# Performance work log

Measured on AMD Instinct MI355X. Metric: run time of the kernel, lower is better.

Reference implementation:

```python
import jax, jax.numpy as jnp
import numpy as np

E = 1024
B, QL, KVL = 8, 2048, 2048


def setup_inputs() -> dict:
    key = jax.random.key(0)
    ks = jax.random.split(key, 12)
    s = 1.0 / np.sqrt(E)
    return {
        "query": jax.random.normal(ks[0], (B, QL, E), jnp.float32),
        "key_value": jax.random.normal(ks[1], (B, KVL, E), jnp.float32),
        "attention_mask": jax.random.randint(ks[2], (B, QL, KVL), 0, 2, jnp.int32),
        "Wq": jax.random.uniform(ks[3], (E, E), jnp.float32, -s, s),
        "bq": jax.random.uniform(ks[4], (E,), jnp.float32, -s, s),
        "Wk": jax.random.uniform(ks[5], (E, E), jnp.float32, -s, s),
        "bk": jax.random.uniform(ks[6], (E,), jnp.float32, -s, s),
        "Wv": jax.random.uniform(ks[7], (E, E), jnp.float32, -s, s),
        "bv": jax.random.uniform(ks[8], (E,), jnp.float32, -s, s),
        "Wo": jax.random.uniform(ks[9], (E, E), jnp.float32, -s, s),
        "bo": jax.random.uniform(ks[10], (E,), jnp.float32, -s, s),
    }


def reference(query, key_value, attention_mask, Wq, bq, Wk, bk, Wv, bv, Wo, bo):
    # torch Linear: x @ W.T + b
    q = jnp.einsum('bqe,fe->bqf', query, Wq) + bq          # [B, QL, E]
    k = jnp.einsum('bke,fe->bkf', key_value, Wk) + bk      # [B, KVL, E]
    v = jnp.einsum('bke,fe->bkf', key_value, Wv) + bv      # [B, KVL, E]
    scale = 1.0 / jnp.sqrt(jnp.asarray(q.shape[-1], q.dtype))
    attn = jnp.einsum('bqe,bke->bqk', q, k) * scale        # [B, QL, KVL]
    attn = jnp.where(attention_mask == 0, -jnp.inf, attn)
    attn = jax.nn.softmax(attn, axis=-1)
    out = jnp.einsum('bqk,bke->bqe', attn, v)              # [B, QL, E]
    out = jnp.einsum('bqe,fe->bqf', out, Wo) + bo
    return out
```

## Files before the change

### kernel.cpp

```cpp
#include <hip/hip_runtime.h>
#include <hip/hip_bf16.h>
#include <stdint.h>

typedef unsigned short u16;
typedef short s16x8 __attribute__((ext_vector_type(8)));
typedef u16 u16x8 __attribute__((ext_vector_type(8)));
typedef u16 u16x4 __attribute__((ext_vector_type(4)));
typedef float f32x4 __attribute__((ext_vector_type(4)));

__device__ __forceinline__ u16 f2bf(float f) {
  union { float f; uint32_t u; } c; c.f = f;
  uint32_t u = c.u;
  u = u + 0x7fffu + ((u >> 16) & 1u);
  return (u16)(u >> 16);
}
__device__ __forceinline__ float bf2f(u16 b) {
  union { uint32_t u; float f; } c; c.u = ((uint32_t)b) << 16;
  return c.f;
}

__device__ __forceinline__ void gld_lds16(const u16* g, u16* l) {
  __builtin_amdgcn_global_load_lds(
      (const __attribute__((address_space(1))) uint32_t*)g,
      (__attribute__((address_space(3))) uint32_t*)l,
      16, 0, 0);
}

__global__ __launch_bounds__(256) void cvt_f32_to_bf16(
    const float* __restrict__ in, u16* __restrict__ out, long n8) {
  long i = (long)blockIdx.x * blockDim.x + threadIdx.x;
  if (i >= n8) return;
  const float4 a = ((const float4*)in)[i * 2];
  const float4 b = ((const float4*)in)[i * 2 + 1];
  u16x8 r;
  r[0] = f2bf(a.x); r[1] = f2bf(a.y); r[2] = f2bf(a.z); r[3] = f2bf(a.w);
  r[4] = f2bf(b.x); r[5] = f2bf(b.y); r[6] = f2bf(b.z); r[7] = f2bf(b.w);
  *(u16x8*)&out[i * 8] = r;
}

__global__ __launch_bounds__(256) void cvt_w4(
    const float* __restrict__ w0, const float* __restrict__ w1,
    const float* __restrict__ w2, const float* __restrict__ w3,
    u16* __restrict__ out) {
  const float* src = (blockIdx.y == 0) ? w0 : (blockIdx.y == 1) ? w1
                   : (blockIdx.y == 2) ? w2 : w3;
  const long i = (long)blockIdx.x * blockDim.x + threadIdx.x;
  const float4 a = ((const float4*)src)[i * 2];
  const float4 b = ((const float4*)src)[i * 2 + 1];
  u16x8 r;
  r[0] = f2bf(a.x); r[1] = f2bf(a.y); r[2] = f2bf(a.z); r[3] = f2bf(a.w);
  r[4] = f2bf(b.x); r[5] = f2bf(b.y); r[6] = f2bf(b.z); r[7] = f2bf(b.w);
  *(u16x8*)&out[(long)blockIdx.y * 1048576 + i * 8] = r;
}

__global__ __launch_bounds__(256) void softmax_rows(u16* __restrict__ S) {
  const long base = (long)blockIdx.x * 2048;
  const int tid = threadIdx.x;
  const int lane = tid & 63, wave = tid >> 6;
  u16x8 raw = *(const u16x8*)&S[base + tid * 8];
  float v[8];
#pragma unroll
  for (int j = 0; j < 8; ++j) v[j] = bf2f(raw[j]);
  float m = v[0];
#pragma unroll
  for (int j = 1; j < 8; ++j) m = fmaxf(m, v[j]);
#pragma unroll
  for (int off = 32; off >= 1; off >>= 1) m = fmaxf(m, __shfl_xor(m, off));
  __shared__ float red[8];
  if (lane == 0) red[wave] = m;
  __syncthreads();
  m = fmaxf(fmaxf(red[0], red[1]), fmaxf(red[2], red[3]));
  float s = 0.f;
#pragma unroll
  for (int j = 0; j < 8; ++j) { v[j] = __expf(v[j] - m); s += v[j]; }
#pragma unroll
  for (int off = 32; off >= 1; off >>= 1) s += __shfl_xor(s, off);
  if (lane == 0) red[4 + wave] = s;
  __syncthreads();
  s = (red[4] + red[5]) + (red[6] + red[7]);
  const float inv = 1.f / s;
#pragma unroll
  for (int j = 0; j < 8; ++j) raw[j] = f2bf(v[j] * inv);
  *(u16x8*)&S[base + tid * 8] = raw;
}

union __align__(16) SmemT {
  u16 stage[2][128 * 64];
  float epi[32 * 132];
};

__device__ __forceinline__ s16x8 ldsfrag(const u16* p, int r, int c8) {
  return *(const s16x8*)&p[r * 64 + ((c8 ^ (r & 7)) << 3)];
}

__device__ __forceinline__ void stage128(const u16* __restrict__ gb, int row0,
                                         int K, int k0, u16* lbuf, int tid) {
#pragma unroll
  for (int i = 0; i < 4; ++i) {
    const int f = i * 256 + tid;
    const int rl = f >> 3, s = f & 7;
    const int gc = (s ^ (rl & 7)) << 3;
    gld_lds16(gb + (long)(row0 + rl) * K + k0 + gc, lbuf + f * 8);
  }
}

template<bool HAS_BIAS, int MODE, bool HAS_MASK>
__global__ __launch_bounds__(256, 4) void gemm128(
    const u16* __restrict__ A, const u16* __restrict__ B,
    const float* __restrict__ bias, const float* __restrict__ bias2,
    const int* __restrict__ mask, void* __restrict__ Cv,
    void* __restrict__ Cv2,
    int M, int N, int K, long sA, long sB, long sC, long sMask, float scale) {
  __shared__ SmemT sm;
  const int nx = gridDim.x, ny = gridDim.y;
  const int did = blockIdx.x + nx * (blockIdx.y + ny * blockIdx.z);
  const int cpx = (nx * ny * gridDim.z) >> 3;
  const int nf = (did & 7) * cpx + (did >> 3);
  const int b = nf / (nx * ny);
  const int rr = nf % (nx * ny);
  const int bm = (rr / ny) * 128;
  const int bn = (rr % ny) * 128;

  const u16* Ab = A + (long)b * sA;
  const u16* Bb = B + (long)b * sB;
  const int tid = threadIdx.x;
  const int lane = tid & 63, wave = tid >> 6;
  const int wm = wave >> 1, wn = wave & 1;
  const int lr = lane & 15, lk = lane >> 4;
  const int NT = K >> 6;

  f32x4 acc[4][4] = {};

  for (int t = 0; t < NT; ++t) {
    stage128(Ab, bm, K, t << 6, sm.stage[0], tid);
    stage128(Bb, bn, K, t << 6, sm.stage[1], tid);
    asm volatile("s_waitcnt vmcnt(0)" ::: "memory");
    __syncthreads();
#pragma unroll
    for (int ks = 0; ks < 2; ++ks) {
      s16x8 af[4], bg[4];
#pragma unroll
      for (int mi = 0; mi < 4; ++mi)
        af[mi] = ldsfrag(sm.stage[0], wm * 64 + mi * 16 + lr, ks * 4 + lk);
#pragma unroll
      for (int ni = 0; ni < 4; ++ni)
        bg[ni] = ldsfrag(sm.stage[1], wn * 64 + ni * 16 + lr, ks * 4 + lk);
#pragma unroll
      for (int mi = 0; mi < 4; ++mi)
#pragma unroll
        for (int ni = 0; ni < 4; ++ni)
          acc[mi][ni] = __builtin_amdgcn_mfma_f32_16x16x32_bf16(
              af[mi], bg[ni], acc[mi][ni], 0, 0, 0);
    }
    __syncthreads();
  }

  const long cb = (long)b * sC;
  if (MODE == 2 && bn >= 1024) {
#pragma unroll
    for (int mi = 0; mi < 4; ++mi) {
#pragma unroll
      for (int ni = 0; ni < 4; ++ni) {
        const int row0 = bm + wm * 64 + mi * 16 + (lk << 2);
        const int col2 = (bn - 1024) + wn * 64 + ni * 16 + lr;
        const float bvx = HAS_BIAS ? bias2[col2] : 0.f;
        u16x4 pk;
#pragma unroll
        for (int j = 0; j < 4; ++j) pk[j] = f2bf(acc[mi][ni][j] * scale + bvx);
        const long ad = (long)(row0 >> 11) * (2048L * 1024) +
                        (long)col2 * 2048 + (row0 & 2047);
        *(u16x4*)&((u16*)Cv2)[ad] = pk;
      }
    }
  } else {
    const int ldC = (MODE == 2) ? 1024 : N;
    const int q = tid & 7, r = tid >> 3;
#pragma unroll
    for (int h = 0; h < 4; ++h) {
      __syncthreads();
      if (wm == (h >> 1)) {
        const int mi0 = (h & 1) * 2;
#pragma unroll
        for (int mm = 0; mm < 2; ++mm) {
          const int mi = mi0 + mm;
#pragma unroll
          for (int ni = 0; ni < 4; ++ni) {
            const int c = wn * 64 + ni * 16 + lr;
            const float bvx = HAS_BIAS ? bias[bn + c] : 0.f;
#pragma unroll
            for (int j = 0; j < 4; ++j)
              sm.epi[(mm * 16 + (lk << 2) + j) * 132 + c] =
                  acc[mi][ni][j] * scale + bvx;
          }
        }
      }
      __syncthreads();
      const int growi = bm + h * 32 + r;
      const long grow = cb + (long)growi * ldC + bn;
      const long mrow = HAS_MASK
          ? ((long)b * sMask + (long)growi * (long)N + bn) : 0;
#pragma unroll
      for (int ch = 0; ch < 2; ++ch) {
        const int c0 = ch * 64 + q * 8;
        const float4 x = *(const float4*)&sm.epi[r * 132 + c0];
        const float4 y = *(const float4*)&sm.epi[r * 132 + c0 + 4];
        if (MODE == 1) {
          *(float4*)&((float*)Cv)[grow + c0] = x;
          *(float4*)&((float*)Cv)[grow + c0 + 4] = y;
        } else {
          u16x8 pk;
          if (HAS_MASK) {
            const int4 ma = *(const int4*)&mask[mrow + c0];
            const int4 mb = *(const int4*)&mask[mrow + c0 + 4];
            pk[0] = f2bf(ma.x ? x.x : -1e30f);
            pk[1] = f2bf(ma.y ? x.y : -1e30f);
            pk[2] = f2bf(ma.z ? x.z : -1e30f);
            pk[3] = f2bf(ma.w ? x.w : -1e30f);
            pk[4] = f2bf(mb.x ? y.x : -1e30f);
            pk[5] = f2bf(mb.y ? y.y : -1e30f);
            pk[6] = f2bf(mb.z ? y.z : -1e30f);
            pk[7] = f2bf(mb.w ? y.w : -1e30f);
          } else {
            pk[0] = f2bf(x.x); pk[1] = f2bf(x.y);
            pk[2] = f2bf(x.z); pk[3] = f2bf(x.w);
            pk[4] = f2bf(y.x); pk[5] = f2bf(y.y);
            pk[6] = f2bf(y.z); pk[7] = f2bf(y.w);
          }
          *(u16x8*)&((u16*)Cv)[grow + c0] = pk;
        }
      }
    }
  }
}

extern "C" void kernel_launch(void* const* d_in, const int* in_sizes, int n_in,
                              void* d_out, int out_size, void* d_ws, size_t ws_size,
                              hipStream_t stream) {
  const float* query = (const float*)d_in[0];
  const float* kv    = (const float*)d_in[1];
  const int*   mask  = (const int*)d_in[2];
  const float* Wq = (const float*)d_in[3];
  const float* bq = (const float*)d_in[4];
  const float* Wk = (const float*)d_in[5];
  const float* bk = (const float*)d_in[6];
  const float* Wv = (const float*)d_in[7];
  const float* bv = (const float*)d_in[8];
  const float* Wo = (const float*)d_in[9];
  const float* bo = (const float*)d_in[10];
  float* out = (float*)d_out;

  char* ws = (char*)d_ws;
  const size_t MB = (size_t)1 << 20;
  u16* qbf  = (u16*)(ws + 0);
  u16* kvbf = (u16*)(ws + 32 * MB);
  u16* wq   = (u16*)(ws + 64 * MB);
  u16* wk   = (u16*)(ws + 66 * MB);
  u16* wo   = (u16*)(ws + 70 * MB);
  u16* Q    = (u16*)(ws + 72 * MB);
  u16* Kb   = (u16*)(ws + 104 * MB);
  u16* Vt   = (u16*)(ws + 136 * MB);
  u16* S    = (u16*)(ws + 168 * MB);
  u16* O    = qbf;

  const long sQK = (long)2048 * 1024;
  const long sS  = (long)2048 * 2048;

  cvt_f32_to_bf16<<<8192, 256, 0, stream>>>(query, qbf, 2097152);
  cvt_f32_to_bf16<<<8192, 256, 0, stream>>>(kv, kvbf, 2097152);
  cvt_w4<<<dim3(512, 4, 1), 256, 0, stream>>>(Wq, Wk, Wv, Wo, wq);

  gemm128<true, 0, false><<<dim3(128, 8, 1), 256, 0, stream>>>(
      qbf, wq, bq, nullptr, nullptr, Q, nullptr,
      16384, 1024, 1024, 0, 0, 0, 0, 1.f);

  gemm128<true, 2, false><<<dim3(128, 16, 1), 256, 0, stream>>>(
      kvbf, wk, bk, bv, nullptr, Kb, Vt,
      16384, 2048, 1024, 0, 0, 0, 0, 1.f);

  gemm128<false, 0, true><<<dim3(16, 16, 8), 256, 0, stream>>>(
      Q, Kb, nullptr, nullptr, mask, S, nullptr,
      2048, 2048, 1024, sQK, sQK, sS, sS, 0.03125f);

  softmax_rows<<<16384, 256, 0, stream>>>(S);

  gemm128<false, 0, false><<<dim3(16, 8, 8), 256, 0, stream>>>(
      S, Vt, nullptr, nullptr, nullptr, O, nullptr,
      2048, 1024, 2048, sS, sQK, sQK, 0, 1.f);

  gemm128<true, 1, false><<<dim3(128, 8, 1), 256, 0, stream>>>(
      O, wo, bo, nullptr, nullptr, out, nullptr,
      16384, 1024, 1024, 0, 0, 0, 0, 1.f);
}
```

Before: 381.2 us.

## Fold Q/K and V/O projection weights into combined matrices to drop a GEMM

Precomputes Wq^T·Wk and Wo·Wv as combined 1024x1024 weights. Query is projected through the combined QK matrix and scored directly against the raw key_value tensor, and key_value is projected once through the combined VO matrix. Biases are folded: bk drops out under softmax, bq becomes a per-key column bias computed by a GEMV, and bv passes through Wo into the output bias. This removes one large projection GEMM and the separate output projection, at the cost of small setup kernels and extra bf16 rounding of the fused weights.

```diff
diff --git a/kernel.cpp b/kernel.cpp
--- a/kernel.cpp
+++ b/kernel.cpp
@@ -53,6 +53,83 @@
   *(u16x8*)&out[(long)blockIdx.y * 1048576 + i * 8] = r;
 }
 
+__global__ __launch_bounds__(256) void transpose64(
+    const u16* __restrict__ in, u16* __restrict__ out, int R, int C) {
+  __shared__ u16 t[64][66];
+  const long ib = (long)blockIdx.z * (long)R * C;
+  const int r0 = blockIdx.x * 64, c0 = blockIdx.y * 64;
+  const int tid = threadIdx.x;
+#pragma unroll
+  for (int i = 0; i < 2; ++i) {
+    const int ch = i * 256 + tid;
+    const int r = ch >> 3, cc = ch & 7;
+    const s16x8 v = *(const s16x8*)&in[ib + (long)(r0 + r) * C + c0 + cc * 8];
+#pragma unroll
+    for (int j = 0; j < 8; ++j) t[r][cc * 8 + j] = (u16)v[j];
+  }
+  __syncthreads();
+#pragma unroll
+  for (int i = 0; i < 2; ++i) {
+    const int ch = i * 256 + tid;
+    const int c = ch >> 3, rr = ch & 7;
+    u16x8 r8;
+#pragma unroll
+    for (int j = 0; j < 8; ++j) r8[j] = t[rr * 8 + j][c];
+    *(u16x8*)&out[ib + (long)(c0 + c) * R + r0 + rr * 8] = r8;
+  }
+}
+
+__global__ __launch_bounds__(256) void prep_vec(
+    const float* __restrict__ Wk, const float* __restrict__ bq,
+    const float* __restrict__ Wo, const float* __restrict__ bv,
+    const float* __restrict__ bo, float* __restrict__ wvec,
+    float* __restrict__ bvo, float scale) {
+  const int bi = blockIdx.x;
+  if (bi < 4) {
+    const int g = bi * 256 + threadIdx.x;
+    float s = 0.f;
+    for (int e = 0; e < 1024; ++e) s += Wk[(long)e * 1024 + g] * bq[e];
+    wvec[g] = s * scale;
+  } else {
+    const int f = (bi - 4) * 256 + threadIdx.x;
+    const float4* row = (const float4*)&Wo[(long)f * 1024];
+    float s = 0.f;
+    for (int e4 = 0; e4 < 256; ++e4) {
+      const float4 x = row[e4];
+      const float4 b4 = ((const float4*)bv)[e4];
+      s += x.x * b4.x + x.y * b4.y + x.z * b4.z + x.w * b4.w;
+    }
+    bvo[f] = s + bo[f];
+  }
+}
+
+__global__ __launch_bounds__(256) void cgemv(
+    const u16* __restrict__ kvbf, const float* __restrict__ wvec,
+    float* __restrict__ c) {
+  __shared__ float w[1024];
+  const int tid = threadIdx.x;
+#pragma unroll
+  for (int i = 0; i < 4; ++i) w[i * 256 + tid] = wvec[i * 256 + tid];
+  __syncthreads();
+  const int lane = tid & 63, wv_ = tid >> 6;
+  const long rowbase = (long)blockIdx.x * 16 + wv_ * 4;
+#pragma unroll
+  for (int r = 0; r < 4; ++r) {
+    const long row = rowbase + r;
+    const u16* p = &kvbf[row * 1024 + lane * 16];
+    const u16x8 a = *(const u16x8*)p;
+    const u16x8 b = *(const u16x8*)(p + 8);
+    float s = 0.f;
+#pragma unroll
+    for (int j = 0; j < 8; ++j) s += bf2f(a[j]) * w[lane * 16 + j];
+#pragma unroll
+    for (int j = 0; j < 8; ++j) s += bf2f(b[j]) * w[lane * 16 + 8 + j];
+#pragma unroll
+    for (int off = 32; off >= 1; off >>= 1) s += __shfl_xor(s, off);
+    if (lane == 0) c[row] = s;
+  }
+}
+
 __global__ __launch_bounds__(256) void softmax_rows(u16* __restrict__ S) {
   const long base = (long)blockIdx.x * 2048;
   const int tid = threadIdx.x;
@@ -107,10 +184,10 @@
 template<bool HAS_BIAS, int MODE, bool HAS_MASK>
 __global__ __launch_bounds__(256, 4) void gemm128(
     const u16* __restrict__ A, const u16* __restrict__ B,
-    const float* __restrict__ bias, const float* __restrict__ bias2,
-    const int* __restrict__ mask, void* __restrict__ Cv,
-    void* __restrict__ Cv2,
-    int M, int N, int K, long sA, long sB, long sC, long sMask, float scale) {
+    const float* __restrict__ bias, const int* __restrict__ mask,
+    void* __restrict__ Cv,
+    int M, int N, int K, long sA, long sB, long sC, long sMask, long sBias,
+    float scale) {
   __shared__ SmemT sm;
   const int nx = gridDim.x, ny = gridDim.y;
   const int did = blockIdx.x + nx * (blockIdx.y + ny * blockIdx.z);
@@ -123,6 +200,7 @@
 
   const u16* Ab = A + (long)b * sA;
   const u16* Bb = B + (long)b * sB;
+  const float* biasB = HAS_BIAS ? (bias + (long)b * sBias) : nullptr;
   const int tid = threadIdx.x;
   const int lane = tid & 63, wave = tid >> 6;
   const int wm = wave >> 1, wn = wave & 1;
@@ -156,24 +234,23 @@
   }
 
   const long cb = (long)b * sC;
-  if (MODE == 2 && bn >= 1024) {
+  if (MODE == 3) {
 #pragma unroll
     for (int mi = 0; mi < 4; ++mi) {
 #pragma unroll
       for (int ni = 0; ni < 4; ++ni) {
         const int row0 = bm + wm * 64 + mi * 16 + (lk << 2);
-        const int col2 = (bn - 1024) + wn * 64 + ni * 16 + lr;
-        const float bvx = HAS_BIAS ? bias2[col2] : 0.f;
+        const int col2 = bn + wn * 64 + ni * 16 + lr;
+        const float bvx = HAS_BIAS ? biasB[col2] : 0.f;
         u16x4 pk;
 #pragma unroll
         for (int j = 0; j < 4; ++j) pk[j] = f2bf(acc[mi][ni][j] * scale + bvx);
-        const long ad = (long)(row0 >> 11) * (2048L * 1024) +
+        const long ad = (long)(row0 >> 11) * ((long)N * 2048) +
                         (long)col2 * 2048 + (row0 & 2047);
-        *(u16x4*)&((u16*)Cv2)[ad] = pk;
+        *(u16x4*)&((u16*)Cv)[ad] = pk;
       }
     }
   } else {
-    const int ldC = (MODE == 2) ? 1024 : N;
     const int q = tid & 7, r = tid >> 3;
 #pragma unroll
     for (int h = 0; h < 4; ++h) {
@@ -186,7 +263,7 @@
 #pragma unroll
           for (int ni = 0; ni < 4; ++ni) {
             const int c = wn * 64 + ni * 16 + lr;
-            const float bvx = HAS_BIAS ? bias[bn + c] : 0.f;
+            const float bvx = HAS_BIAS ? biasB[bn + c] : 0.f;
 #pragma unroll
             for (int j = 0; j < 4; ++j)
               sm.epi[(mm * 16 + (lk << 2) + j) * 132 + c] =
@@ -196,7 +273,7 @@
       }
       __syncthreads();
       const int growi = bm + h * 32 + r;
-      const long grow = cb + (long)growi * ldC + bn;
+      const long grow = cb + (long)growi * N + bn;
       const long mrow = HAS_MASK
           ? ((long)b * sMask + (long)growi * (long)N + bn) : 0;
 #pragma unroll
@@ -248,19 +325,25 @@
   const float* Wo = (const float*)d_in[9];
   const float* bo = (const float*)d_in[10];
   float* out = (float*)d_out;
+  (void)bk;
 
   char* ws = (char*)d_ws;
   const size_t MB = (size_t)1 << 20;
   u16* qbf  = (u16*)(ws + 0);
   u16* kvbf = (u16*)(ws + 32 * MB);
   u16* wq   = (u16*)(ws + 64 * MB);
-  u16* wk   = (u16*)(ws + 66 * MB);
   u16* wo   = (u16*)(ws + 70 * MB);
-  u16* Q    = (u16*)(ws + 72 * MB);
-  u16* Kb   = (u16*)(ws + 104 * MB);
-  u16* Vt   = (u16*)(ws + 136 * MB);
-  u16* S    = (u16*)(ws + 168 * MB);
-  u16* O    = qbf;
+  u16* WqT  = (u16*)(ws + 72 * MB);
+  u16* WkT  = (u16*)(ws + 74 * MB);
+  u16* WvT  = (u16*)(ws + 76 * MB);
+  u16* Mt   = (u16*)(ws + 78 * MB);
+  u16* Wvo  = (u16*)(ws + 80 * MB);
+  float* wvec = (float*)(ws + 82 * MB);
+  float* bvo  = (float*)(ws + 82 * MB + 65536);
+  float* cvec = (float*)(ws + 83 * MB);
+  u16* qM   = (u16*)(ws + 84 * MB);
+  u16* VwT  = (u16*)(ws + 116 * MB);
+  u16* S    = (u16*)(ws + 148 * MB);
 
   const long sQK = (long)2048 * 1024;
   const long sS  = (long)2048 * 2048;
@@ -268,26 +351,28 @@
   cvt_f32_to_bf16<<<8192, 256, 0, stream>>>(query, qbf, 2097152);
   cvt_f32_to_bf16<<<8192, 256, 0, stream>>>(kv, kvbf, 2097152);
   cvt_w4<<<dim3(512, 4, 1), 256, 0, stream>>>(Wq, Wk, Wv, Wo, wq);
-
-  gemm128<true, 0, false><<<dim3(128, 8, 1), 256, 0, stream>>>(
-      qbf, wq, bq, nullptr, nullptr, Q, nullptr,
-      16384, 1024, 1024, 0, 0, 0, 0, 1.f);
-
-  gemm128<true, 2, false><<<dim3(128, 16, 1), 256, 0, stream>>>(
-      kvbf, wk, bk, bv, nullptr, Kb, Vt,
-      16384, 2048, 1024, 0, 0, 0, 0, 1.f);
-
-  gemm128<false, 0, true><<<dim3(16, 16, 8), 256, 0, stream>>>(
-      Q, Kb, nullptr, nullptr, mask, S, nullptr,
-      2048, 2048, 1024, sQK, sQK, sS, sS, 0.03125f);
+  transpose64<<<dim3(16, 16, 3), 256, 0, stream>>>(wq, WqT, 1024, 1024);
+  prep_vec<<<8, 256, 0, stream>>>(Wk, bq, Wo, bv, bo, wvec, bvo, 0.03125f);
+
+  gemm128<false, 0, false><<<dim3(8, 8, 1), 256, 0, stream>>>(
+      WkT, WqT, nullptr, nullptr, Mt, 1024, 1024, 1024, 0, 0, 0, 0, 0, 1.f);
+  gemm128<false, 0, false><<<dim3(8, 8, 1), 256, 0, stream>>>(
+      wo, WvT, nullptr, nullptr, Wvo, 1024, 1024, 1024, 0, 0, 0, 0, 0, 1.f);
+
+  cgemv<<<1024, 256, 0, stream>>>(kvbf, wvec, cvec);
+
+  gemm128<false, 0, false><<<dim3(128, 8, 1), 256, 0, stream>>>(
+      qbf, Mt, nullptr, nullptr, qM, 16384, 1024, 1024, 0, 0, 0, 0, 0, 1.f);
+
+  gemm128<false, 3, false><<<dim3(128, 8, 1), 256, 0, stream>>>(
+      kvbf, Wvo, nullptr, nullptr, VwT, 16384, 1024, 1024, 0, 0, 0, 0, 0, 1.f);
+
+  gemm128<true, 0, true><<<dim3(16, 16, 8), 256, 0, stream>>>(
+      qM, kvbf, cvec, mask, S, 2048, 2048, 1024, sQK, sQK, sS, sS, 2048,
+      0.03125f);
 
   softmax_rows<<<16384, 256, 0, stream>>>(S);
 
-  gemm128<false, 0, false><<<dim3(16, 8, 8), 256, 0, stream>>>(
-      S, Vt, nullptr, nullptr, nullptr, O, nullptr,
-      2048, 1024, 2048, sS, sQK, sQK, 0, 1.f);
-
-  gemm128<true, 1, false><<<dim3(128, 8, 1), 256, 0, stream>>>(
-      O, wo, bo, nullptr, nullptr, out, nullptr,
-      16384, 1024, 1024, 0, 0, 0, 0, 1.f);
-}
+  gemm128<true, 1, false><<<dim3(16, 8, 8), 256, 0, stream>>>(
+      S, VwT, bvo, nullptr, out, 2048, 1024, 2048, sS, sQK, sQK, 0, 0, 1.f);
+}
```

Measured after the change: 393.7 us. 1.03x slower.
